# Kernel optimization log

Hardware: AMD Instinct MI355X
Metric: run time of the kernel (lower is better)

## Reference

```python
import jax, jax.numpy as jnp
import numpy as np

ATOM_FDIM = 35
BOND_FDIM = 5
MAX_NB = 10
HIDDEN = 128
DEPTH = 6
A = 131072   # total atoms
B = 262144   # total directed bonds
M = 32768    # tree messages (row 0 is the zero pad vector, as in the torch code)
N_MOLS = 4096


def setup_inputs() -> dict:
    key = jax.random.key(0)
    ks = jax.random.split(key, 9)
    atom_feats = jax.random.uniform(ks[0], (A, ATOM_FDIM), dtype=jnp.float32)
    bond_feats = jax.random.uniform(ks[1], (B, ATOM_FDIM + BOND_FDIM), dtype=jnp.float32)
    tree_message = jax.random.normal(ks[2], (M, HIDDEN), dtype=jnp.float32)
    tree_message = tree_message.at[0].set(0.0)  # all_mess[0] = zeros padding
    atom_graph = jax.random.randint(ks[3], (A, MAX_NB), 0, M + B)
    bond_graph = jax.random.randint(ks[4], (B, MAX_NB), 0, M + B)
    s = 1.0 / np.sqrt(HIDDEN)
    W_i = jax.random.uniform(ks[5], (HIDDEN, ATOM_FDIM + BOND_FDIM), jnp.float32, -s, s)
    W_h = jax.random.uniform(ks[6], (HIDDEN, HIDDEN), jnp.float32, -s, s)
    W_o = jax.random.uniform(ks[7], (HIDDEN, ATOM_FDIM + HIDDEN), jnp.float32, -s, s)
    b_o = jax.random.uniform(ks[8], (HIDDEN,), jnp.float32, -s, s)
    return {"atom_feats": atom_feats, "bond_feats": bond_feats,
            "tree_message": tree_message, "atom_graph": atom_graph,
            "bond_graph": bond_graph, "n_mols": N_MOLS,
            "W_i": W_i, "W_h": W_h, "W_o": W_o, "b_o": b_o}


def reference(atom_feats, bond_feats, tree_message, atom_graph, bond_graph,
              n_mols, W_i, W_h, W_o, b_o):
    # h0 = ReLU(W_i @ bond_feats): [B, H]
    h0 = jax.nn.relu(jnp.einsum('bf,hf->bh', bond_feats, W_i))
    graph_message = h0
    for _ in range(DEPTH - 1):
        message = jnp.concatenate([tree_message, graph_message], axis=0)  # [M+B, H]
        nei = jnp.take(message, bond_graph, axis=0).sum(axis=1)           # [B, H]
        graph_message = jax.nn.relu(h0 + jnp.einsum('bh,gh->bg', nei, W_h))
    message = jnp.concatenate([tree_message, graph_message], axis=0)
    nei_a = jnp.take(message, atom_graph, axis=0).sum(axis=1)             # [A, H]
    atom_in = jnp.concatenate([atom_feats, nei_a], axis=1)                # [A, F+H]
    atom_hiddens = jax.nn.relu(jnp.einsum('af,hf->ah', atom_in, W_o) + b_o)
    # per-molecule mean over equal-size contiguous scopes
    atoms_per_mol = A // n_mols
    mol_ids = jnp.arange(A) // atoms_per_mol
    mol_vecs = jax.ops.segment_sum(atom_hiddens, mol_ids, num_segments=n_mols)
    return mol_vecs / atoms_per_mol
```

## Files before the change

kernel.cpp:

```cpp
#include <hip/hip_runtime.h>

#define H       128
#define MAXNB   10
#define M_TREE  32768
#define NBOND   262144
#define NATOM   131072
#define FATOM   35
#define FBOND   40
#define FOUT    163
#define KPAD    192
#define NMOLS   4096
#define APM     32
#define TB      64
#define TA      64

typedef __bf16 bf16x8 __attribute__((ext_vector_type(8)));
typedef float  f32x4  __attribute__((ext_vector_type(4)));
typedef unsigned int u32x4 __attribute__((ext_vector_type(4)));

__device__ __forceinline__ unsigned short f32_to_bf16(float f) {
  unsigned int u = __float_as_uint(f);
  u += 0x7FFFu + ((u >> 16) & 1u);
  return (unsigned short)(u >> 16);
}
__device__ __forceinline__ float bf16u_to_f32(unsigned short h) {
  return __uint_as_float(((unsigned int)h) << 16);
}
__device__ __forceinline__ unsigned int bfpair_addrelu(unsigned int a, unsigned int h) {
  float a0 = __uint_as_float(a << 16), a1 = __uint_as_float(a & 0xFFFF0000u);
  float h0v = __uint_as_float(h << 16), h1v = __uint_as_float(h & 0xFFFF0000u);
  float r0 = fmaxf(a0 + h0v, 0.f), r1 = fmaxf(a1 + h1v, 0.f);
  return ((unsigned int)f32_to_bf16(r1) << 16) | (unsigned int)f32_to_bf16(r0);
}

__global__ __launch_bounds__(256) void prep(const float* __restrict__ tm,
                                            const float* __restrict__ wh,
                                            const float* __restrict__ wo,
                                            const float* __restrict__ wi,
                                            unsigned short* __restrict__ tmsg,
                                            unsigned short* __restrict__ whb,
                                            unsigned short* __restrict__ wob,
                                            unsigned short* __restrict__ wib) {
  int i = blockIdx.x * 256 + threadIdx.x;
  const int n1 = M_TREE * H;
  const int n2 = H * H;
  const int n3 = H * KPAD;
  const int n4 = H * 64;
  if (i < n1) { tmsg[i] = f32_to_bf16(__builtin_nontemporal_load(tm + i)); return; }
  int j = i - n1;
  if (j < n2) { whb[j] = f32_to_bf16(wh[j]); return; }
  int k = j - n2;
  if (k < n3) {
    int g = k / KPAD, kk = k - g * KPAD;
    float v = 0.f;
    if (kk < 35)                   v = wo[g * FOUT + kk];
    else if (kk >= 36 && kk < 164) v = wo[g * FOUT + kk - 1];
    wob[k] = f32_to_bf16(v);
    return;
  }
  int m = k - n3;
  if (m < n4) {
    int g = m / 64, kk = m - g * 64;
    wib[m] = (kk < FBOND) ? f32_to_bf16(wi[g * FBOND + kk]) : (unsigned short)0;
  }
}

__global__ __launch_bounds__(256, 3) void wi_gemm(const float* __restrict__ bond_feats,
                                                  const unsigned short* __restrict__ wib,
                                                  unsigned short* __restrict__ h0) {
  __shared__ unsigned short sF[128][72];
  const int t = threadIdx.x;
  const int lane = t & 63;
  const int wave = t >> 6;
  const int n16 = lane & 15;
  const int quad = lane >> 4;
  const int b0 = blockIdx.x * 128;

  for (int i = t; i < 128 * FBOND; i += 256) {
    int b = i / FBOND, f = i - b * FBOND;
    sF[b][f] = f32_to_bf16(__builtin_nontemporal_load(bond_feats + b0 * FBOND + i));
  }
  for (int i = t; i < 128 * 24; i += 256) {
    int b = i / 24, c = 40 + i - b * 24;
    sF[b][c] = 0;
  }
  bf16x8 Bf[2][2];
#pragma unroll
  for (int kt = 0; kt < 2; ++kt)
#pragma unroll
    for (int nt = 0; nt < 2; ++nt)
      Bf[kt][nt] = *(const bf16x8*)(wib + ((wave * 2 + nt) * 16 + n16) * 64 + kt * 32 + quad * 8);
  __syncthreads();

  f32x4 acc[8][2];
  f32x4 zero = {0.f, 0.f, 0.f, 0.f};
#pragma unroll
  for (int mt = 0; mt < 8; ++mt) { acc[mt][0] = zero; acc[mt][1] = zero; }
#pragma unroll
  for (int kt = 0; kt < 2; ++kt)
#pragma unroll
    for (int mt = 0; mt < 8; ++mt) {
      bf16x8 av = *(const bf16x8*)&sF[mt * 16 + n16][kt * 32 + quad * 8];
      acc[mt][0] = __builtin_amdgcn_mfma_f32_16x16x32_bf16(av, Bf[kt][0], acc[mt][0], 0, 0, 0);
      acc[mt][1] = __builtin_amdgcn_mfma_f32_16x16x32_bf16(av, Bf[kt][1], acc[mt][1], 0, 0, 0);
    }
#pragma unroll
  for (int mt = 0; mt < 8; ++mt)
#pragma unroll
    for (int nt = 0; nt < 2; ++nt) {
      const int col = (wave * 2 + nt) * 16 + n16;
#pragma unroll
      for (int r = 0; r < 4; ++r) {
        const int b = b0 + mt * 16 + quad * 4 + r;
        h0[b * H + col] = f32_to_bf16(fmaxf(acc[mt][nt][r], 0.f));
      }
    }
}

__global__ __launch_bounds__(256, 6) void mp_step(const unsigned short* __restrict__ gm_in,
                                                  unsigned short* __restrict__ gm_out,
                                                  const unsigned short* __restrict__ h0,
                                                  const unsigned short* __restrict__ tmsg,
                                                  const int* __restrict__ bond_graph,
                                                  const unsigned short* __restrict__ whb) {
  __shared__ unsigned short snei[TB][136];
  __shared__ int sBG[TB * MAXNB];
  const int t = threadIdx.x;
  const int lane = t & 63;
  const int wave = t >> 6;
  const int n16 = lane & 15;
  const int quad = lane >> 4;
  const int b0 = blockIdx.x * TB;

  for (int i = t; i < TB * MAXNB; i += 256) sBG[i] = bond_graph[b0 * MAXNB + i];
  __syncthreads();

  const unsigned short* gsh = gm_in - (size_t)M_TREE * H;
  for (int lb = wave * 4; lb < TB; lb += 16) {
    unsigned int u[4][MAXNB];
#pragma unroll
    for (int p = 0; p < 4; ++p) {
      const int* ig = &sBG[(lb + p) * MAXNB];
#pragma unroll
      for (int j = 0; j < MAXNB; ++j) {
        int idx = __builtin_amdgcn_readfirstlane(ig[j]);
        const unsigned short* r = ((idx < M_TREE) ? tmsg : gsh) + (size_t)idx * H;
        u[p][j] = *(const unsigned int*)(r + 2 * lane);
      }
    }
#pragma unroll
    for (int p = 0; p < 4; ++p) {
      float a0 = 0.f, a1 = 0.f;
#pragma unroll
      for (int j = 0; j < MAXNB; ++j) {
        a0 += __uint_as_float(u[p][j] << 16);
        a1 += __uint_as_float(u[p][j] & 0xFFFF0000u);
      }
      unsigned int packed = ((unsigned int)f32_to_bf16(a1) << 16) | (unsigned int)f32_to_bf16(a0);
      *(unsigned int*)&snei[lb + p][2 * lane] = packed;
    }
  }

  bf16x8 Bf[4][2];
#pragma unroll
  for (int kt = 0; kt < 4; ++kt)
#pragma unroll
    for (int nt = 0; nt < 2; ++nt)
      Bf[kt][nt] = *(const bf16x8*)(whb + ((wave * 2 + nt) * 16 + n16) * H + kt * 32 + quad * 8);
  __syncthreads();

  f32x4 acc[4][2];
  f32x4 zero = {0.f, 0.f, 0.f, 0.f};
#pragma unroll
  for (int mt = 0; mt < 4; ++mt) { acc[mt][0] = zero; acc[mt][1] = zero; }
#pragma unroll
  for (int kt = 0; kt < 4; ++kt)
#pragma unroll
    for (int mt = 0; mt < 4; ++mt) {
      bf16x8 av = *(const bf16x8*)&snei[mt * 16 + n16][kt * 32 + quad * 8];
      acc[mt][0] = __builtin_amdgcn_mfma_f32_16x16x32_bf16(av, Bf[kt][0], acc[mt][0], 0, 0, 0);
      acc[mt][1] = __builtin_amdgcn_mfma_f32_16x16x32_bf16(av, Bf[kt][1], acc[mt][1], 0, 0, 0);
    }
  __syncthreads();

#pragma unroll
  for (int mt = 0; mt < 4; ++mt)
#pragma unroll
    for (int nt = 0; nt < 2; ++nt) {
      const int col = (wave * 2 + nt) * 16 + n16;
#pragma unroll
      for (int r = 0; r < 4; ++r)
        snei[mt * 16 + quad * 4 + r][col] = f32_to_bf16(acc[mt][nt][r]);
    }
  __syncthreads();

  const size_t gbase = (size_t)b0 * H;
#pragma unroll
  for (int c = 0; c < 4; ++c) {
    int fl = c * 256 + t;
    int row = fl >> 4;
    int col = (fl & 15) * 8;
    u32x4 a4 = *(const u32x4*)&snei[row][col];
    u32x4 h4 = *(const u32x4*)(h0 + gbase + (size_t)row * H + col);
    u32x4 o4;
    o4.x = bfpair_addrelu(a4.x, h4.x);
    o4.y = bfpair_addrelu(a4.y, h4.y);
    o4.z = bfpair_addrelu(a4.z, h4.z);
    o4.w = bfpair_addrelu(a4.w, h4.w);
    *(u32x4*)(gm_out + gbase + (size_t)row * H + col) = o4;
  }
}

__global__ __launch_bounds__(256, 4) void readout(const float* __restrict__ atom_feats,
                                                  const unsigned short* __restrict__ gm,
                                                  const unsigned short* __restrict__ tmsg,
                                                  const int* __restrict__ atom_graph,
                                                  const unsigned short* __restrict__ wob,
                                                  const float* __restrict__ b_o,
                                                  float* __restrict__ out) {
  __shared__ unsigned short sA[TA][200];
  __shared__ int sAG[TA * MAXNB];
  const int t = threadIdx.x;
  const int lane = t & 63;
  const int wave = t >> 6;
  const int n16 = lane & 15;
  const int quad = lane >> 4;
  const int blk = blockIdx.x;
  const int abase = blk * TA;

  for (int i = t; i < TA * MAXNB; i += 256)
    sAG[i] = __builtin_nontemporal_load(atom_graph + abase * MAXNB + i);
  for (int i = t; i < TA * FATOM; i += 256) {
    int a = i / FATOM, f = i - a * FATOM;
    sA[a][f] = f32_to_bf16(__builtin_nontemporal_load(atom_feats + abase * FATOM + i));
  }
  if (t < TA) sA[t][35] = 0;
  for (int i = t; i < TA * 28; i += 256) {
    int a = i / 28, c = 164 + i - a * 28;
    sA[a][c] = 0;
  }
  __syncthreads();

  const unsigned short* gsh = gm - (size_t)M_TREE * H;
  for (int la = wave * 4; la < TA; la += 16) {
    unsigned int u[4][MAXNB];
#pragma unroll
    for (int p = 0; p < 4; ++p) {
      const int* ig = &sAG[(la + p) * MAXNB];
#pragma unroll
      for (int j = 0; j < MAXNB; ++j) {
        int idx = __builtin_amdgcn_readfirstlane(ig[j]);
        const unsigned short* r = ((idx < M_TREE) ? tmsg : gsh) + (size_t)idx * H;
        u[p][j] = *(const unsigned int*)(r + 2 * lane);
      }
    }
#pragma unroll
    for (int p = 0; p < 4; ++p) {
      float a0 = 0.f, a1 = 0.f;
#pragma unroll
      for (int j = 0; j < MAXNB; ++j) {
        a0 += __uint_as_float(u[p][j] << 16);
        a1 += __uint_as_float(u[p][j] & 0xFFFF0000u);
      }
      unsigned int packed = ((unsigned int)f32_to_bf16(a1) << 16) | (unsigned int)f32_to_bf16(a0);
      *(unsigned int*)&sA[la + p][36 + 2 * lane] = packed;
    }
  }

  bf16x8 Bf[6][2];
#pragma unroll
  for (int kt = 0; kt < 6; ++kt)
#pragma unroll
    for (int nt = 0; nt < 2; ++nt)
      Bf[kt][nt] = *(const bf16x8*)(wob + ((wave * 2 + nt) * 16 + n16) * KPAD + kt * 32 + quad * 8);
  __syncthreads();

  f32x4 acc[4][2];
  f32x4 zero = {0.f, 0.f, 0.f, 0.f};
#pragma unroll
  for (int mt = 0; mt < 4; ++mt) { acc[mt][0] = zero; acc[mt][1] = zero; }
#pragma unroll
  for (int kt = 0; kt < 6; ++kt)
#pragma unroll
    for (int mt = 0; mt < 4; ++mt) {
      bf16x8 av = *(const bf16x8*)&sA[mt * 16 + n16][kt * 32 + quad * 8];
      acc[mt][0] = __builtin_amdgcn_mfma_f32_16x16x32_bf16(av, Bf[kt][0], acc[mt][0], 0, 0, 0);
      acc[mt][1] = __builtin_amdgcn_mfma_f32_16x16x32_bf16(av, Bf[kt][1], acc[mt][1], 0, 0, 0);
    }

  float bo[2] = { b_o[(wave * 2) * 16 + n16], b_o[(wave * 2 + 1) * 16 + n16] };
  float part[2][2] = {{0.f,0.f},{0.f,0.f}};
#pragma unroll
  for (int mt = 0; mt < 4; ++mt)
#pragma unroll
    for (int nt = 0; nt < 2; ++nt)
#pragma unroll
      for (int r = 0; r < 4; ++r)
        part[mt >> 1][nt] += fmaxf(acc[mt][nt][r] + bo[nt], 0.f);
#pragma unroll
  for (int mol = 0; mol < 2; ++mol)
#pragma unroll
    for (int nt = 0; nt < 2; ++nt) {
      float p = part[mol][nt];
      p += __shfl_xor(p, 16);
      p += __shfl_xor(p, 32);
      if (lane < 16)
        out[(blk * 2 + mol) * H + (wave * 2 + nt) * 16 + lane] = p * (1.0f / APM);
    }
}

extern "C" void kernel_launch(void* const* d_in, const int* in_sizes, int n_in,
                              void* d_out, int out_size, void* d_ws, size_t ws_size,
                              hipStream_t stream) {
  (void)in_sizes; (void)n_in; (void)out_size; (void)ws_size;
  const float* atom_feats   = (const float*)d_in[0];
  const float* bond_feats   = (const float*)d_in[1];
  const float* tree_message = (const float*)d_in[2];
  const int*   atom_graph   = (const int*)d_in[3];
  const int*   bond_graph   = (const int*)d_in[4];
  const float* W_i = (const float*)d_in[6];
  const float* W_h = (const float*)d_in[7];
  const float* W_o = (const float*)d_in[8];
  const float* b_o = (const float*)d_in[9];
  float* out = (float*)d_out;

  char* ws = (char*)d_ws;
  unsigned short* tmsg = (unsigned short*)(ws);
  unsigned short* whb  = (unsigned short*)(ws + 8388608);
  unsigned short* wob  = (unsigned short*)(ws + 8421376);
  unsigned short* wib  = (unsigned short*)(ws + 8470528);
  unsigned short* h0   = (unsigned short*)(ws + 8486912);
  unsigned short* gm0  = (unsigned short*)(ws + 75595776);
  unsigned short* gm1  = (unsigned short*)(ws + 142704640);

  prep<<<16576, 256, 0, stream>>>(tree_message, W_h, W_o, W_i, tmsg, whb, wob, wib);
  wi_gemm<<<NBOND / 128, 256, 0, stream>>>(bond_feats, wib, h0);
  mp_step<<<NBOND / TB, 256, 0, stream>>>(h0,  gm0, h0, tmsg, bond_graph, whb);
  mp_step<<<NBOND / TB, 256, 0, stream>>>(gm0, gm1, h0, tmsg, bond_graph, whb);
  mp_step<<<NBOND / TB, 256, 0, stream>>>(gm1, gm0, h0, tmsg, bond_graph, whb);
  mp_step<<<NBOND / TB, 256, 0, stream>>>(gm0, gm1, h0, tmsg, bond_graph, whb);
  mp_step<<<NBOND / TB, 256, 0, stream>>>(gm1, gm0, h0, tmsg, bond_graph, whb);
  readout<<<NATOM / TA, 256, 0, stream>>>(atom_feats, gm0, tmsg, atom_graph, wob, b_o, out);
}
```

Measured before the change: 762.6 us.

## Store bond messages in bitmask-compressed sparse rows to cut gather bandwidth

```diff
diff --git a/kernel.cpp b/kernel.cpp
--- a/kernel.cpp
+++ b/kernel.cpp
@@ -13,6 +13,7 @@
 #define APM     32
 #define TB      64
 #define TA      64
+#define CSTRIDE 160
 
 typedef __bf16 bf16x8 __attribute__((ext_vector_type(8)));
 typedef float  f32x4  __attribute__((ext_vector_type(4)));
@@ -26,11 +27,59 @@
 __device__ __forceinline__ float bf16u_to_f32(unsigned short h) {
   return __uint_as_float(((unsigned int)h) << 16);
 }
-__device__ __forceinline__ unsigned int bfpair_addrelu(unsigned int a, unsigned int h) {
-  float a0 = __uint_as_float(a << 16), a1 = __uint_as_float(a & 0xFFFF0000u);
-  float h0v = __uint_as_float(h << 16), h1v = __uint_as_float(h & 0xFFFF0000u);
-  float r0 = fmaxf(a0 + h0v, 0.f), r1 = fmaxf(a1 + h1v, 0.f);
-  return ((unsigned int)f32_to_bf16(r1) << 16) | (unsigned int)f32_to_bf16(r0);
+
+__device__ __forceinline__ unsigned long long mort2(unsigned int e, unsigned int o) {
+  unsigned long long x = e, y = o;
+  x = (x | (x << 16)) & 0x0000FFFF0000FFFFull;
+  x = (x | (x << 8))  & 0x00FF00FF00FF00FFull;
+  x = (x | (x << 4))  & 0x0F0F0F0F0F0F0F0Full;
+  x = (x | (x << 2))  & 0x3333333333333333ull;
+  x = (x | (x << 1))  & 0x5555555555555555ull;
+  y = (y | (y << 16)) & 0x0000FFFF0000FFFFull;
+  y = (y | (y << 8))  & 0x00FF00FF00FF00FFull;
+  y = (y | (y << 4))  & 0x0F0F0F0F0F0F0F0Full;
+  y = (y | (y << 2))  & 0x3333333333333333ull;
+  y = (y | (y << 1))  & 0x5555555555555555ull;
+  return x | (y << 1);
+}
+
+__device__ __forceinline__ unsigned int crow_read(const unsigned short* __restrict__ rp, int li) {
+  u32x4 h = *(const u32x4*)rp;
+  unsigned long long bm0 = (unsigned long long)h.x | ((unsigned long long)h.y << 32);
+  unsigned long long bm1 = (unsigned long long)h.z | ((unsigned long long)h.w << 32);
+  const bool hi = li >= 32;
+  unsigned long long bm = hi ? bm1 : bm0;
+  int base = hi ? (int)__popcll(bm0) : 0;
+  int sh = (li & 31) * 2;
+  int pos = base + (int)__popcll(bm & ((1ull << sh) - 1ull));
+  unsigned int p0 = (unsigned int)((bm >> sh) & 1ull);
+  unsigned int p1 = (unsigned int)((bm >> (sh + 1)) & 1ull);
+  unsigned short w0 = rp[8 + pos];
+  unsigned short w1 = rp[8 + pos + 1];
+  unsigned short v0 = p0 ? w0 : (unsigned short)0;
+  unsigned short v1 = p1 ? (p0 ? w1 : w0) : (unsigned short)0;
+  return (unsigned int)v0 | ((unsigned int)v1 << 16);
+}
+
+__device__ __forceinline__ void crow_write(unsigned short* __restrict__ wp, int li,
+                                           unsigned short v0, unsigned short v1) {
+  unsigned long long be = __ballot(v0 != 0);
+  unsigned long long bo = __ballot(v1 != 0);
+  unsigned long long obm0 = mort2((unsigned int)be, (unsigned int)bo);
+  unsigned long long obm1 = mort2((unsigned int)(be >> 32), (unsigned int)(bo >> 32));
+  const bool hi = li >= 32;
+  unsigned long long obm = hi ? obm1 : obm0;
+  int base = hi ? (int)__popcll(obm0) : 0;
+  int sh = (li & 31) * 2;
+  int pos = base + (int)__popcll(obm & ((1ull << sh) - 1ull));
+  if (li == 0) {
+    u32x4 hd;
+    hd.x = (unsigned int)obm0; hd.y = (unsigned int)(obm0 >> 32);
+    hd.z = (unsigned int)obm1; hd.w = (unsigned int)(obm1 >> 32);
+    *(u32x4*)wp = hd;
+  }
+  if (v0) wp[8 + pos] = v0;
+  if (v1) wp[8 + pos + (v0 ? 1 : 0)] = v1;
 }
 
 __global__ __launch_bounds__(256) void prep(const float* __restrict__ tm,
@@ -65,22 +114,23 @@
   }
 }
 
-__global__ __launch_bounds__(256, 3) void wi_gemm(const float* __restrict__ bond_feats,
+__global__ __launch_bounds__(256, 4) void wi_gemm(const float* __restrict__ bond_feats,
                                                   const unsigned short* __restrict__ wib,
-                                                  unsigned short* __restrict__ h0) {
-  __shared__ unsigned short sF[128][72];
+                                                  unsigned short* __restrict__ ch0) {
+  __shared__ unsigned short sF[64][72];
+  __shared__ unsigned short sStage[64][136];
   const int t = threadIdx.x;
   const int lane = t & 63;
   const int wave = t >> 6;
   const int n16 = lane & 15;
   const int quad = lane >> 4;
-  const int b0 = blockIdx.x * 128;
-
-  for (int i = t; i < 128 * FBOND; i += 256) {
+  const int b0 = blockIdx.x * 64;
+
+  for (int i = t; i < 64 * FBOND; i += 256) {
     int b = i / FBOND, f = i - b * FBOND;
     sF[b][f] = f32_to_bf16(__builtin_nontemporal_load(bond_feats + b0 * FBOND + i));
   }
-  for (int i = t; i < 128 * 24; i += 256) {
+  for (int i = t; i < 64 * 24; i += 256) {
     int b = i / 24, c = 40 + i - b * 24;
     sF[b][c] = 0;
   }
@@ -92,34 +142,38 @@
       Bf[kt][nt] = *(const bf16x8*)(wib + ((wave * 2 + nt) * 16 + n16) * 64 + kt * 32 + quad * 8);
   __syncthreads();
 
-  f32x4 acc[8][2];
+  f32x4 acc[4][2];
   f32x4 zero = {0.f, 0.f, 0.f, 0.f};
 #pragma unroll
-  for (int mt = 0; mt < 8; ++mt) { acc[mt][0] = zero; acc[mt][1] = zero; }
+  for (int mt = 0; mt < 4; ++mt) { acc[mt][0] = zero; acc[mt][1] = zero; }
 #pragma unroll
   for (int kt = 0; kt < 2; ++kt)
 #pragma unroll
-    for (int mt = 0; mt < 8; ++mt) {
+    for (int mt = 0; mt < 4; ++mt) {
       bf16x8 av = *(const bf16x8*)&sF[mt * 16 + n16][kt * 32 + quad * 8];
       acc[mt][0] = __builtin_amdgcn_mfma_f32_16x16x32_bf16(av, Bf[kt][0], acc[mt][0], 0, 0, 0);
       acc[mt][1] = __builtin_amdgcn_mfma_f32_16x16x32_bf16(av, Bf[kt][1], acc[mt][1], 0, 0, 0);
     }
 #pragma unroll
-  for (int mt = 0; mt < 8; ++mt)
+  for (int mt = 0; mt < 4; ++mt)
 #pragma unroll
     for (int nt = 0; nt < 2; ++nt) {
       const int col = (wave * 2 + nt) * 16 + n16;
 #pragma unroll
-      for (int r = 0; r < 4; ++r) {
-        const int b = b0 + mt * 16 + quad * 4 + r;
-        h0[b * H + col] = f32_to_bf16(fmaxf(acc[mt][nt][r], 0.f));
-      }
-    }
-}
-
-__global__ __launch_bounds__(256, 6) void mp_step(const unsigned short* __restrict__ gm_in,
-                                                  unsigned short* __restrict__ gm_out,
-                                                  const unsigned short* __restrict__ h0,
+      for (int r = 0; r < 4; ++r)
+        sStage[mt * 16 + quad * 4 + r][col] = f32_to_bf16(fmaxf(acc[mt][nt][r], 0.f));
+    }
+  __syncthreads();
+  for (int r = wave; r < 64; r += 4) {
+    unsigned int a = *(const unsigned int*)&sStage[r][2 * lane];
+    crow_write(ch0 + (size_t)(b0 + r) * CSTRIDE, lane,
+               (unsigned short)a, (unsigned short)(a >> 16));
+  }
+}
+
+__global__ __launch_bounds__(256, 5) void mp_step(const unsigned short* __restrict__ gin,
+                                                  unsigned short* __restrict__ gout,
+                                                  const unsigned short* __restrict__ ch0,
                                                   const unsigned short* __restrict__ tmsg,
                                                   const int* __restrict__ bond_graph,
                                                   const unsigned short* __restrict__ whb) {
@@ -135,26 +189,22 @@
   for (int i = t; i < TB * MAXNB; i += 256) sBG[i] = bond_graph[b0 * MAXNB + i];
   __syncthreads();
 
-  const unsigned short* gsh = gm_in - (size_t)M_TREE * H;
-  for (int lb = wave * 4; lb < TB; lb += 16) {
-    unsigned int u[4][MAXNB];
-#pragma unroll
-    for (int p = 0; p < 4; ++p) {
+  for (int lb = wave * 2; lb < TB; lb += 8) {
+#pragma unroll
+    for (int p = 0; p < 2; ++p) {
       const int* ig = &sBG[(lb + p) * MAXNB];
+      float a0 = 0.f, a1 = 0.f;
 #pragma unroll
       for (int j = 0; j < MAXNB; ++j) {
         int idx = __builtin_amdgcn_readfirstlane(ig[j]);
-        const unsigned short* r = ((idx < M_TREE) ? tmsg : gsh) + (size_t)idx * H;
-        u[p][j] = *(const unsigned int*)(r + 2 * lane);
-      }
-    }
-#pragma unroll
-    for (int p = 0; p < 4; ++p) {
-      float a0 = 0.f, a1 = 0.f;
-#pragma unroll
-      for (int j = 0; j < MAXNB; ++j) {
-        a0 += __uint_as_float(u[p][j] << 16);
-        a1 += __uint_as_float(u[p][j] & 0xFFFF0000u);
+        unsigned int u;
+        if (idx < M_TREE) {
+          u = *(const unsigned int*)(tmsg + (size_t)idx * H + 2 * lane);
+        } else {
+          u = crow_read(gin + (size_t)(idx - M_TREE) * CSTRIDE, lane);
+        }
+        a0 += __uint_as_float(u << 16);
+        a1 += __uint_as_float(u & 0xFFFF0000u);
       }
       unsigned int packed = ((unsigned int)f32_to_bf16(a1) << 16) | (unsigned int)f32_to_bf16(a0);
       *(unsigned int*)&snei[lb + p][2 * lane] = packed;
@@ -194,20 +244,12 @@
     }
   __syncthreads();
 
-  const size_t gbase = (size_t)b0 * H;
-#pragma unroll
-  for (int c = 0; c < 4; ++c) {
-    int fl = c * 256 + t;
-    int row = fl >> 4;
-    int col = (fl & 15) * 8;
-    u32x4 a4 = *(const u32x4*)&snei[row][col];
-    u32x4 h4 = *(const u32x4*)(h0 + gbase + (size_t)row * H + col);
-    u32x4 o4;
-    o4.x = bfpair_addrelu(a4.x, h4.x);
-    o4.y = bfpair_addrelu(a4.y, h4.y);
-    o4.z = bfpair_addrelu(a4.z, h4.z);
-    o4.w = bfpair_addrelu(a4.w, h4.w);
-    *(u32x4*)(gm_out + gbase + (size_t)row * H + col) = o4;
+  for (int r = wave; r < TB; r += 4) {
+    unsigned int a = *(const unsigned int*)&snei[r][2 * lane];
+    unsigned int hh = crow_read(ch0 + (size_t)(b0 + r) * CSTRIDE, lane);
+    float v0f = fmaxf(bf16u_to_f32((unsigned short)hh) + bf16u_to_f32((unsigned short)a), 0.f);
+    float v1f = fmaxf(bf16u_to_f32((unsigned short)(hh >> 16)) + bf16u_to_f32((unsigned short)(a >> 16)), 0.f);
+    crow_write(gout + (size_t)(b0 + r) * CSTRIDE, lane, f32_to_bf16(v0f), f32_to_bf16(v1f));
   }
 }
 
@@ -241,26 +283,22 @@
   }
   __syncthreads();
 
-  const unsigned short* gsh = gm - (size_t)M_TREE * H;
-  for (int la = wave * 4; la < TA; la += 16) {
-    unsigned int u[4][MAXNB];
-#pragma unroll
-    for (int p = 0; p < 4; ++p) {
+  for (int la = wave * 2; la < TA; la += 8) {
+#pragma unroll
+    for (int p = 0; p < 2; ++p) {
       const int* ig = &sAG[(la + p) * MAXNB];
+      float a0 = 0.f, a1 = 0.f;
 #pragma unroll
       for (int j = 0; j < MAXNB; ++j) {
         int idx = __builtin_amdgcn_readfirstlane(ig[j]);
-        const unsigned short* r = ((idx < M_TREE) ? tmsg : gsh) + (size_t)idx * H;
-        u[p][j] = *(const unsigned int*)(r + 2 * lane);
-      }
-    }
-#pragma unroll
-    for (int p = 0; p < 4; ++p) {
-      float a0 = 0.f, a1 = 0.f;
-#pragma unroll
-      for (int j = 0; j < MAXNB; ++j) {
-        a0 += __uint_as_float(u[p][j] << 16);
-        a1 += __uint_as_float(u[p][j] & 0xFFFF0000u);
+        unsigned int u;
+        if (idx < M_TREE) {
+          u = *(const unsigned int*)(tmsg + (size_t)idx * H + 2 * lane);
+        } else {
+          u = crow_read(gm + (size_t)(idx - M_TREE) * CSTRIDE, lane);
+        }
+        a0 += __uint_as_float(u << 16);
+        a1 += __uint_as_float(u & 0xFFFF0000u);
       }
       unsigned int packed = ((unsigned int)f32_to_bf16(a1) << 16) | (unsigned int)f32_to_bf16(a0);
       *(unsigned int*)&sA[la + p][36 + 2 * lane] = packed;
@@ -329,16 +367,16 @@
   unsigned short* whb  = (unsigned short*)(ws + 8388608);
   unsigned short* wob  = (unsigned short*)(ws + 8421376);
   unsigned short* wib  = (unsigned short*)(ws + 8470528);
-  unsigned short* h0   = (unsigned short*)(ws + 8486912);
-  unsigned short* gm0  = (unsigned short*)(ws + 75595776);
-  unsigned short* gm1  = (unsigned short*)(ws + 142704640);
+  unsigned short* ch0  = (unsigned short*)(ws + 8486912);
+  unsigned short* gmc0 = (unsigned short*)(ws + 92372992);
+  unsigned short* gmc1 = (unsigned short*)(ws + 176259072);
 
   prep<<<16576, 256, 0, stream>>>(tree_message, W_h, W_o, W_i, tmsg, whb, wob, wib);
-  wi_gemm<<<NBOND / 128, 256, 0, stream>>>(bond_feats, wib, h0);
-  mp_step<<<NBOND / TB, 256, 0, stream>>>(h0,  gm0, h0, tmsg, bond_graph, whb);
-  mp_step<<<NBOND / TB, 256, 0, stream>>>(gm0, gm1, h0, tmsg, bond_graph, whb);
-  mp_step<<<NBOND / TB, 256, 0, stream>>>(gm1, gm0, h0, tmsg, bond_graph, whb);
-  mp_step<<<NBOND / TB, 256, 0, stream>>>(gm0, gm1, h0, tmsg, bond_graph, whb);
-  mp_step<<<NBOND / TB, 256, 0, stream>>>(gm1, gm0, h0, tmsg, bond_graph, whb);
-  readout<<<NATOM / TA, 256, 0, stream>>>(atom_feats, gm0, tmsg, atom_graph, wob, b_o, out);
-}
+  wi_gemm<<<NBOND / 64, 256, 0, stream>>>(bond_feats, wib, ch0);
+  mp_step<<<NBOND / TB, 256, 0, stream>>>(ch0,  gmc0, ch0, tmsg, bond_graph, whb);
+  mp_step<<<NBOND / TB, 256, 0, stream>>>(gmc0, gmc1, ch0, tmsg, bond_graph, whb);
+  mp_step<<<NBOND / TB, 256, 0, stream>>>(gmc1, gmc0, ch0, tmsg, bond_graph, whb);
+  mp_step<<<NBOND / TB, 256, 0, stream>>>(gmc0, gmc1, ch0, tmsg, bond_graph, whb);
+  mp_step<<<NBOND / TB, 256, 0, stream>>>(gmc1, gmc0, ch0, tmsg, bond_graph, whb);
+  readout<<<NATOM / TA, 256, 0, stream>>>(atom_feats, gmc0, tmsg, atom_graph, wob, b_o, out);
+}
```

New measurement: 2.277 ms. 2.99x slower.

## Recompute h0 in each message step from padded bf16 bond features

Applied to the files above, without the earlier changes.

```diff
diff --git a/kernel.cpp b/kernel.cpp
--- a/kernel.cpp
+++ b/kernel.cpp
@@ -26,26 +26,23 @@
 __device__ __forceinline__ float bf16u_to_f32(unsigned short h) {
   return __uint_as_float(((unsigned int)h) << 16);
 }
-__device__ __forceinline__ unsigned int bfpair_addrelu(unsigned int a, unsigned int h) {
-  float a0 = __uint_as_float(a << 16), a1 = __uint_as_float(a & 0xFFFF0000u);
-  float h0v = __uint_as_float(h << 16), h1v = __uint_as_float(h & 0xFFFF0000u);
-  float r0 = fmaxf(a0 + h0v, 0.f), r1 = fmaxf(a1 + h1v, 0.f);
-  return ((unsigned int)f32_to_bf16(r1) << 16) | (unsigned int)f32_to_bf16(r0);
-}
 
 __global__ __launch_bounds__(256) void prep(const float* __restrict__ tm,
                                             const float* __restrict__ wh,
                                             const float* __restrict__ wo,
                                             const float* __restrict__ wi,
+                                            const float* __restrict__ bf,
                                             unsigned short* __restrict__ tmsg,
                                             unsigned short* __restrict__ whb,
                                             unsigned short* __restrict__ wob,
-                                            unsigned short* __restrict__ wib) {
+                                            unsigned short* __restrict__ wib,
+                                            unsigned short* __restrict__ bfb) {
   int i = blockIdx.x * 256 + threadIdx.x;
   const int n1 = M_TREE * H;
   const int n2 = H * H;
   const int n3 = H * KPAD;
   const int n4 = H * 64;
+  const int n5 = NBOND * 64;
   if (i < n1) { tmsg[i] = f32_to_bf16(__builtin_nontemporal_load(tm + i)); return; }
   int j = i - n1;
   if (j < n2) { whb[j] = f32_to_bf16(wh[j]); return; }
@@ -62,10 +59,17 @@
   if (m < n4) {
     int g = m / 64, kk = m - g * 64;
     wib[m] = (kk < FBOND) ? f32_to_bf16(wi[g * FBOND + kk]) : (unsigned short)0;
-  }
-}
-
-__global__ __launch_bounds__(256, 3) void wi_gemm(const float* __restrict__ bond_feats,
+    return;
+  }
+  int q = m - n4;
+  if (q < n5) {
+    int b = q >> 6, kk = q & 63;
+    bfb[q] = (kk < FBOND) ? f32_to_bf16(__builtin_nontemporal_load(bf + b * FBOND + kk))
+                          : (unsigned short)0;
+  }
+}
+
+__global__ __launch_bounds__(256, 3) void wi_gemm(const unsigned short* __restrict__ bfb,
                                                   const unsigned short* __restrict__ wib,
                                                   unsigned short* __restrict__ h0) {
   __shared__ unsigned short sF[128][72];
@@ -76,13 +80,12 @@
   const int quad = lane >> 4;
   const int b0 = blockIdx.x * 128;
 
-  for (int i = t; i < 128 * FBOND; i += 256) {
-    int b = i / FBOND, f = i - b * FBOND;
-    sF[b][f] = f32_to_bf16(__builtin_nontemporal_load(bond_feats + b0 * FBOND + i));
-  }
-  for (int i = t; i < 128 * 24; i += 256) {
-    int b = i / 24, c = 40 + i - b * 24;
-    sF[b][c] = 0;
+#pragma unroll
+  for (int c = 0; c < 4; ++c) {
+    int fl = c * 256 + t;
+    int row = fl >> 3, q = fl & 7;
+    *(u32x4*)&sF[row][q * 8] =
+        *(const u32x4*)(bfb + (size_t)(b0 + row) * 64 + q * 8);
   }
   bf16x8 Bf[2][2];
 #pragma unroll
@@ -117,13 +120,15 @@
     }
 }
 
-__global__ __launch_bounds__(256, 6) void mp_step(const unsigned short* __restrict__ gm_in,
-                                                  unsigned short* __restrict__ gm_out,
-                                                  const unsigned short* __restrict__ h0,
+__global__ __launch_bounds__(256, 5) void mp_step(const unsigned short* __restrict__ gin,
+                                                  unsigned short* __restrict__ gout,
                                                   const unsigned short* __restrict__ tmsg,
                                                   const int* __restrict__ bond_graph,
-                                                  const unsigned short* __restrict__ whb) {
+                                                  const unsigned short* __restrict__ whb,
+                                                  const unsigned short* __restrict__ wib,
+                                                  const unsigned short* __restrict__ bfb) {
   __shared__ unsigned short snei[TB][136];
+  __shared__ unsigned short sBF[TB][72];
   __shared__ int sBG[TB * MAXNB];
   const int t = threadIdx.x;
   const int lane = t & 63;
@@ -133,13 +138,20 @@
   const int b0 = blockIdx.x * TB;
 
   for (int i = t; i < TB * MAXNB; i += 256) sBG[i] = bond_graph[b0 * MAXNB + i];
-  __syncthreads();
-
-  const unsigned short* gsh = gm_in - (size_t)M_TREE * H;
-  for (int lb = wave * 4; lb < TB; lb += 16) {
-    unsigned int u[4][MAXNB];
-#pragma unroll
-    for (int p = 0; p < 4; ++p) {
+#pragma unroll
+  for (int c = 0; c < 2; ++c) {
+    int fl = c * 256 + t;
+    int row = fl >> 3, q = fl & 7;
+    *(u32x4*)&sBF[row][q * 8] =
+        *(const u32x4*)(bfb + (size_t)(b0 + row) * 64 + q * 8);
+  }
+  __syncthreads();
+
+  const unsigned short* gsh = gin - (size_t)M_TREE * H;
+  for (int lb = wave * 2; lb < TB; lb += 8) {
+    unsigned int u[2][MAXNB];
+#pragma unroll
+    for (int p = 0; p < 2; ++p) {
       const int* ig = &sBG[(lb + p) * MAXNB];
 #pragma unroll
       for (int j = 0; j < MAXNB; ++j) {
@@ -149,7 +161,7 @@
       }
     }
 #pragma unroll
-    for (int p = 0; p < 4; ++p) {
+    for (int p = 0; p < 2; ++p) {
       float a0 = 0.f, a1 = 0.f;
 #pragma unroll
       for (int j = 0; j < MAXNB; ++j) {
@@ -161,6 +173,37 @@
     }
   }
 
+  f32x4 zero = {0.f, 0.f, 0.f, 0.f};
+  unsigned int h0p[4][2][2];
+  {
+    bf16x8 Bfi[2][2];
+#pragma unroll
+    for (int kt = 0; kt < 2; ++kt)
+#pragma unroll
+      for (int nt = 0; nt < 2; ++nt)
+        Bfi[kt][nt] = *(const bf16x8*)(wib + ((wave * 2 + nt) * 16 + n16) * 64 + kt * 32 + quad * 8);
+    f32x4 acci[4][2];
+#pragma unroll
+    for (int mt = 0; mt < 4; ++mt) { acci[mt][0] = zero; acci[mt][1] = zero; }
+#pragma unroll
+    for (int kt = 0; kt < 2; ++kt)
+#pragma unroll
+      for (int mt = 0; mt < 4; ++mt) {
+        bf16x8 av = *(const bf16x8*)&sBF[mt * 16 + n16][kt * 32 + quad * 8];
+        acci[mt][0] = __builtin_amdgcn_mfma_f32_16x16x32_bf16(av, Bfi[kt][0], acci[mt][0], 0, 0, 0);
+        acci[mt][1] = __builtin_amdgcn_mfma_f32_16x16x32_bf16(av, Bfi[kt][1], acci[mt][1], 0, 0, 0);
+      }
+#pragma unroll
+    for (int mt = 0; mt < 4; ++mt)
+#pragma unroll
+      for (int nt = 0; nt < 2; ++nt) {
+        h0p[mt][nt][0] = (unsigned int)f32_to_bf16(fmaxf(acci[mt][nt][0], 0.f)) |
+                         ((unsigned int)f32_to_bf16(fmaxf(acci[mt][nt][1], 0.f)) << 16);
+        h0p[mt][nt][1] = (unsigned int)f32_to_bf16(fmaxf(acci[mt][nt][2], 0.f)) |
+                         ((unsigned int)f32_to_bf16(fmaxf(acci[mt][nt][3], 0.f)) << 16);
+      }
+  }
+
   bf16x8 Bf[4][2];
 #pragma unroll
   for (int kt = 0; kt < 4; ++kt)
@@ -170,7 +213,6 @@
   __syncthreads();
 
   f32x4 acc[4][2];
-  f32x4 zero = {0.f, 0.f, 0.f, 0.f};
 #pragma unroll
   for (int mt = 0; mt < 4; ++mt) { acc[mt][0] = zero; acc[mt][1] = zero; }
 #pragma unroll
@@ -189,8 +231,11 @@
     for (int nt = 0; nt < 2; ++nt) {
       const int col = (wave * 2 + nt) * 16 + n16;
 #pragma unroll
-      for (int r = 0; r < 4; ++r)
-        snei[mt * 16 + quad * 4 + r][col] = f32_to_bf16(acc[mt][nt][r]);
+      for (int r = 0; r < 4; ++r) {
+        unsigned int hp = h0p[mt][nt][r >> 1];
+        float hv = bf16u_to_f32((unsigned short)((r & 1) ? (hp >> 16) : hp));
+        snei[mt * 16 + quad * 4 + r][col] = f32_to_bf16(fmaxf(hv + acc[mt][nt][r], 0.f));
+      }
     }
   __syncthreads();
 
@@ -200,14 +245,7 @@
     int fl = c * 256 + t;
     int row = fl >> 4;
     int col = (fl & 15) * 8;
-    u32x4 a4 = *(const u32x4*)&snei[row][col];
-    u32x4 h4 = *(const u32x4*)(h0 + gbase + (size_t)row * H + col);
-    u32x4 o4;
-    o4.x = bfpair_addrelu(a4.x, h4.x);
-    o4.y = bfpair_addrelu(a4.y, h4.y);
-    o4.z = bfpair_addrelu(a4.z, h4.z);
-    o4.w = bfpair_addrelu(a4.w, h4.w);
-    *(u32x4*)(gm_out + gbase + (size_t)row * H + col) = o4;
+    *(u32x4*)(gout + gbase + (size_t)row * H + col) = *(const u32x4*)&snei[row][col];
   }
 }
 
@@ -242,10 +280,10 @@
   __syncthreads();
 
   const unsigned short* gsh = gm - (size_t)M_TREE * H;
-  for (int la = wave * 4; la < TA; la += 16) {
-    unsigned int u[4][MAXNB];
-#pragma unroll
-    for (int p = 0; p < 4; ++p) {
+  for (int la = wave * 2; la < TA; la += 8) {
+    unsigned int u[2][MAXNB];
+#pragma unroll
+    for (int p = 0; p < 2; ++p) {
       const int* ig = &sAG[(la + p) * MAXNB];
 #pragma unroll
       for (int j = 0; j < MAXNB; ++j) {
@@ -255,7 +293,7 @@
       }
     }
 #pragma unroll
-    for (int p = 0; p < 4; ++p) {
+    for (int p = 0; p < 2; ++p) {
       float a0 = 0.f, a1 = 0.f;
 #pragma unroll
       for (int j = 0; j < MAXNB; ++j) {
@@ -329,16 +367,18 @@
   unsigned short* whb  = (unsigned short*)(ws + 8388608);
   unsigned short* wob  = (unsigned short*)(ws + 8421376);
   unsigned short* wib  = (unsigned short*)(ws + 8470528);
-  unsigned short* h0   = (unsigned short*)(ws + 8486912);
-  unsigned short* gm0  = (unsigned short*)(ws + 75595776);
-  unsigned short* gm1  = (unsigned short*)(ws + 142704640);
-
-  prep<<<16576, 256, 0, stream>>>(tree_message, W_h, W_o, W_i, tmsg, whb, wob, wib);
-  wi_gemm<<<NBOND / 128, 256, 0, stream>>>(bond_feats, wib, h0);
-  mp_step<<<NBOND / TB, 256, 0, stream>>>(h0,  gm0, h0, tmsg, bond_graph, whb);
-  mp_step<<<NBOND / TB, 256, 0, stream>>>(gm0, gm1, h0, tmsg, bond_graph, whb);
-  mp_step<<<NBOND / TB, 256, 0, stream>>>(gm1, gm0, h0, tmsg, bond_graph, whb);
-  mp_step<<<NBOND / TB, 256, 0, stream>>>(gm0, gm1, h0, tmsg, bond_graph, whb);
-  mp_step<<<NBOND / TB, 256, 0, stream>>>(gm1, gm0, h0, tmsg, bond_graph, whb);
+  unsigned short* bfb  = (unsigned short*)(ws + 8486912);
+  unsigned short* h0   = (unsigned short*)(ws + 42041344);
+  unsigned short* gm0  = (unsigned short*)(ws + 109150208);
+  unsigned short* gm1  = (unsigned short*)(ws + 176259072);
+
+  prep<<<82112, 256, 0, stream>>>(tree_message, W_h, W_o, W_i, bond_feats,
+                                  tmsg, whb, wob, wib, bfb);
+  wi_gemm<<<NBOND / 128, 256, 0, stream>>>(bfb, wib, h0);
+  mp_step<<<NBOND / TB, 256, 0, stream>>>(h0,  gm0, tmsg, bond_graph, whb, wib, bfb);
+  mp_step<<<NBOND / TB, 256, 0, stream>>>(gm0, gm1, tmsg, bond_graph, whb, wib, bfb);
+  mp_step<<<NBOND / TB, 256, 0, stream>>>(gm1, gm0, tmsg, bond_graph, whb, wib, bfb);
+  mp_step<<<NBOND / TB, 256, 0, stream>>>(gm0, gm1, tmsg, bond_graph, whb, wib, bfb);
+  mp_step<<<NBOND / TB, 256, 0, stream>>>(gm1, gm0, tmsg, bond_graph, whb, wib, bfb);
   readout<<<NATOM / TA, 256, 0, stream>>>(atom_feats, gm0, tmsg, atom_graph, wob, b_o, out);
 }
```

New measurement: 819.9 us. 1.08x slower.
